# Performance work log

Measured on AMD Instinct MI355X. Metric: run time of the kernel, lower is better.

## Reference

```python
import jax, jax.numpy as jnp
import numpy as np

B, C, H, W = 16, 64, 64, 64
HD = 128


def skew(x):
    # x: [B,C,H,W] -> [B,C,H,H+W-1], row r shifted right by r
    b, c, h, w = x.shape
    sw = h + w - 1
    xp = jnp.pad(x, ((0, 0), (0, 0), (0, 0), (0, h - 1)))
    cols = (jnp.arange(sw)[None, :] - jnp.arange(h)[:, None]) % sw  # [H,SW]
    return xp[:, :, jnp.arange(h)[:, None], cols]


def unskew(x):
    # x: [B,C,H,SW] -> [B,C,H,W]
    b, c, h, sw = x.shape
    w = sw - h + 1
    cols = jnp.arange(w)[None, :] + jnp.arange(h)[:, None]  # [H,W]
    return x[:, :, jnp.arange(h)[:, None], cols]


def setup_inputs() -> dict:
    key = jax.random.key(0)
    k1, k2, k3, k4, k5 = jax.random.split(key, 5)
    s_is = 1.0 / np.sqrt(C)
    s_ss = 1.0 / np.sqrt(HD * 2)
    return {
        "x": jax.random.normal(k1, (B, C, H, W), jnp.float32),
        "w_is": jax.random.uniform(k2, (5 * HD, C), jnp.float32, -s_is, s_is),   # 1x1 conv (mask B, k=1 => plain)
        "b_is": jax.random.uniform(k3, (5 * HD,), jnp.float32, -s_is, s_is),
        "w_ss": jax.random.uniform(k4, (5 * HD, HD, 2), jnp.float32, -s_ss, s_ss),  # Conv1d k=2
        "b_ss": jax.random.uniform(k5, (5 * HD,), jnp.float32, -s_ss, s_ss),
    }


def reference(x, w_is, b_is, w_ss, b_ss):
    hd = w_ss.shape[1]
    sk = skew(x)  # [B,C,H,SW]
    # input-to-state: 1x1 conv over skewed map
    i_s = jnp.einsum("oc,bchw->bohw", w_is, sk) + b_is[None, :, None, None]
    is_cols = jnp.moveaxis(i_s, -1, 0)  # [SW,B,5hd,H]
    w0, w1 = w_ss[:, :, 0], w_ss[:, :, 1]  # taps for h[t-1], h[t]
    bsz, h_dim = x.shape[0], x.shape[2]

    def step(carry, ic):
        h_prev, c_prev = carry
        h_sh = jnp.pad(h_prev, ((0, 0), (0, 0), (1, 0)))[:, :, :-1]
        s_s = (jnp.einsum("oi,bih->boh", w1, h_prev)
               + jnp.einsum("oi,bih->boh", w0, h_sh)
               + b_ss[None, :, None])
        gates = ic + s_s
        o, fl, fu, i, g = jnp.split(gates, 5, axis=1)
        o, fl, fu, i = map(jax.nn.sigmoid, (o, fl, fu, i))
        g = jnp.tanh(g)
        c_sh = jnp.pad(c_prev, ((0, 0), (0, 0), (1, 0)))[:, :, :-1]
        c = fl * c_prev + fu * c_sh + i * g
        h = o * jnp.tanh(c)
        return (h, c), h

    z = jnp.zeros((bsz, hd, h_dim), x.dtype)
    _, hs = jax.lax.scan(step, (z, z), is_cols)
    hs = jnp.moveaxis(hs, 0, -1)  # [B,hd,H,SW]
    return unskew(hs)
```

## Files before the change

kernel.cpp:

```cpp
#include <hip/hip_runtime.h>

typedef __attribute__((ext_vector_type(8))) short bf16x8;
typedef __attribute__((ext_vector_type(4))) float f32x4;
typedef __attribute__((ext_vector_type(4))) uint  u32x4;

#define B_   16
#define C_   64
#define H_   64
#define W_   64
#define HD_  128
#define K_   320
#define SW_  127

#define NG    4
#define GH    32
#define NCG   64
#define TC    16
#define NT    640
#define ROWS  160
#define NKT   10
#define GPS   17

#define HSLOT  131072LL
#define CBX    524288LL
#define CNT    557056LL
#define GCNT   559104LL
#define AFB    561152LL
#define AF_N   204800LL
#define XT     765952LL
#define XT_N   4194304LL
#define WS_MIN (AFB + AF_N)
#define WS_XT  (XT + XT_N)

#define POLL_CAP (1 << 20)

__device__ __forceinline__ float sigm(float v) { return 1.f / (1.f + __expf(-v)); }
__device__ __forceinline__ float tanh_fast(float v) {
    float e = __expf(2.f * v);
    return 1.f - 2.f / (e + 1.f);
}

__device__ __forceinline__ int rload(int* p) {
    return __hip_atomic_load(p, __ATOMIC_RELAXED, __HIP_MEMORY_SCOPE_AGENT);
}
__device__ __forceinline__ void rbump(int* p) {
    __hip_atomic_fetch_add(p, 1, __ATOMIC_RELAXED, __HIP_MEMORY_SCOPE_AGENT);
}
__device__ __forceinline__ void wait_ge(int* p, int tgt) {
    int guard = 0;
    while (rload(p) < tgt) { if (++guard > POLL_CAP) break; }
    __atomic_signal_fence(__ATOMIC_ACQUIRE);
}

__device__ __forceinline__ void stu_nw(uint* p, uint v) {
    asm volatile("global_store_dword %0, %1, off sc0 sc1" :: "v"(p), "v"(v) : "memory");
}

__device__ __forceinline__ void poll2(const uint* p0, const uint* p1, uint want,
                                      u32x4& A, u32x4& B) {
    int guard = 0;
    while (true) {
        u32x4 a, b;
        asm volatile("global_load_dwordx4 %0, %2, off sc0 sc1\n\t"
                     "global_load_dwordx4 %1, %3, off sc0 sc1\n\t"
                     "s_waitcnt vmcnt(0)"
                     : "=&v"(a), "=&v"(b) : "v"(p0), "v"(p1) : "memory");
        uint m = a[0] & a[1] & a[2] & a[3] & b[0] & b[1] & b[2] & b[3];
        uint o = a[0] | a[1] | a[2] | a[3] | b[0] | b[1] | b[2] | b[3];
        bool ok = want ? ((m & 1u) != 0u) : ((o & 1u) == 0u);
        if (ok || ++guard > POLL_CAP) { A = a; B = b; return; }
    }
}
__device__ __forceinline__ void poll1(const uint* p, uint want, u32x4& A) {
    int guard = 0;
    while (true) {
        u32x4 a;
        asm volatile("global_load_dwordx4 %0, %1, off sc0 sc1\n\ts_waitcnt vmcnt(0)"
                     : "=&v"(a) : "v"(p) : "memory");
        uint m = a[0] & a[1] & a[2] & a[3];
        uint o = a[0] | a[1] | a[2] | a[3];
        bool ok = want ? ((m & 1u) != 0u) : ((o & 1u) == 0u);
        if (ok || ++guard > POLL_CAP) { A = a; return; }
    }
}

__device__ __forceinline__ uint bf16hi(uint u) { return (u + 0x7FFFu + ((u >> 16) & 1u)) >> 16; }
__device__ __forceinline__ uint2 splitbf(float v) {
    uint uh = bf16hi(__float_as_uint(v));
    float rl = v - __uint_as_float(uh << 16);
    uint ul = bf16hi(__float_as_uint(rl));
    return make_uint2(uh, ul);
}

__global__ void lstm_prep(const float* __restrict__ w_is,
                          const float* __restrict__ w_ss,
                          float* __restrict__ ws, long long n_ws)
{
    const long long stride = (long long)gridDim.x * blockDim.x;
    const long long t0 = (long long)blockIdx.x * blockDim.x + threadIdx.x;
    uint* wsu = (uint*)ws;

    for (long long i = t0; i < 524288LL + 32768LL; i += stride) {
        long long a = (i < 524288LL) ? i : (CBX + (i - 524288LL));
        stu_nw(wsu + a, 0x00000001u);
    }
    for (long long i = CNT + t0; i < CNT + 4096; i += stride)
        stu_nw(wsu + i, 0u);

    if (n_ws >= WS_MIN) {
        ushort* af = (ushort*)(ws + AFB);
        for (long long e = t0; e < AF_N; e += stride) {
            int idx   = (int)e;
            int chunk = idx >> 9;
            int lane  = (idx >> 3) & 63;
            int jj    = idx & 7;
            int g  = chunk / (10 * NKT);
            int rm = chunk % (10 * NKT);
            int rt = rm / NKT, kt = rm % NKT;
            int m = lane & 15, quad = lane >> 4;
            int r = rt * 16 + m;
            int q = r >> 5, hl = r & 31;
            int o = q * HD_ + g * GH + hl;
            int k = kt * 32 + quad * 8 + jj;
            float v;
            if (k < C_)            v = w_is[o * C_ + k];
            else if (k < C_ + HD_) v = w_ss[(o * HD_ + (k - C_)) * 2 + 1];
            else                   v = w_ss[(o * HD_ + (k - C_ - HD_)) * 2 + 0];
            uint uh = bf16hi(__float_as_uint(v));
            float rl = v - __uint_as_float(uh << 16);
            uint ul = bf16hi(__float_as_uint(rl));
            int base = chunk * 1024 + lane * 16 + jj;
            af[base]     = (ushort)uh;
            af[base + 8] = (ushort)ul;
        }
    }
}

__global__ void lstm_xpose(const float* __restrict__ x, float* __restrict__ ws)
{
    __shared__ float L[64 * 65];
    const int b = blockIdx.x >> 6, hr = blockIdx.x & 63;
    const int tid = threadIdx.x;
    #pragma unroll
    for (int it = 0; it < 16; ++it) {
        int c = it * 4 + (tid >> 6), w = tid & 63;
        L[c * 65 + w] = x[(((size_t)b * C_ + c) * H_ + hr) * W_ + w];
    }
    __syncthreads();
    float* xt = ws + XT;
    #pragma unroll
    for (int it = 0; it < 16; ++it) {
        int w = it * 4 + (tid >> 6), c = tid & 63;
        xt[(((size_t)b * H_ + hr) * W_ + w) * C_ + c] = L[c * 65 + w];
    }
}

__global__ void __launch_bounds__(NT, 3) lstm_persist(
    const float* __restrict__ x,
    const float* __restrict__ ws_c,
    const float* __restrict__ b_is,
    const float* __restrict__ b_ss,
    float* __restrict__ out,
    float* __restrict__ ws,
    int use_xt)
{
    __shared__ uint  Bf[NKT * 576];
    __shared__ float Gp[ROWS * GPS];
    __shared__ float Cs[2][17 * GH];
    __shared__ float bias_s[ROWS];

    const int tid = threadIdx.x;
    const int cgp = blockIdx.x >> 2;
    const int g   = blockIdx.x & 3;
    const int n0  = cgp * TC;
    const int inb  = (n0 & 63) != 0;
    const int hasr = ((n0 + TC) & 63) != 0;

    uint* hring = (uint*)ws;
    uint* cring = (uint*)(ws + CBX);
    int*  gcntp = (int*)(ws + GCNT);
    const float* xt = ws_c + XT;
    const uint4* afq = (const uint4*)(ws_c + AFB);

    if (tid < ROWS) {
        int q = tid >> 5, hl = tid & 31;
        int o = q * HD_ + g * GH + hl;
        bias_s[tid] = b_is[o] + b_ss[o];
    }
    if (tid < 17 * GH) Cs[0][tid] = 0.f;
    if (tid >= 544 && tid < 544 + GH) Cs[1][tid - 544] = 0.f;

    const int lane = tid & 63;
    const int wv   = tid >> 6;
    const int quad = lane >> 4;
    const int colc = lane & 15;
    uint* bfr = &Bf[lane * 8 + ((lane >> 2) << 2)];
    const uint4* ap0 = afq + (size_t)((g * 10 + wv) * NKT) * 128 + lane * 2;

    const int wkt = (wv < 8) ? (wv + 2) : (wv - 8);
    uint* wp = bfr + wkt * 576;
    int hn = 0, hd0 = 0, hskip = 0;
    if (wv < 8) {
        if (wv < 4) { hn = n0 + colc;     hd0 = wv * 32 + quad * 8; }
        else        { hn = n0 - 1 + colc; hd0 = (wv - 4) * 32 + quad * 8;
                      hskip = (colc == 0 && !inb); }
    }
    const int xc0 = (wv >= 8) ? ((wv - 8) * 32 + quad * 8) : 0;
    const int xn = n0 + colc, xb = xn >> 6, xhr = xn & 63;
    const int ii = tid - 512;

    bf16x8 Ahr[NKT], Alr[NKT];
    #pragma unroll
    for (int kt = 0; kt < NKT; ++kt) {
        uint4 ha = ap0[kt * 128];
        Ahr[kt] = *(bf16x8*)&ha;
        asm volatile("" : "+v"(Ahr[kt]));
        uint4 la = ap0[kt * 128 + 1];
        Alr[kt] = *(bf16x8*)&la;
        asm volatile("" : "+v"(Alr[kt]));
    }

    __syncthreads();

    for (int j = 0; j < SW_; ++j) {
        const uint want = ((j - 1) >> 2) & 1u;
        const uint wtag = (j >> 2) & 1u;

        if (wv < 8) {
            u32x4 a = {0, 0, 0, 0}, b = {0, 0, 0, 0};
            if (j > 0 && !hskip) {
                const uint* p = hring + (size_t)((j - 1) & 3) * HSLOT + hn * 128 + hd0;
                poll2(p, p + 4, want, a, b);
            }
            float hv8[8];
            #pragma unroll
            for (int r = 0; r < 4; ++r) {
                hv8[r]     = __uint_as_float(a[r]);
                hv8[4 + r] = __uint_as_float(b[r]);
            }
            uint hw[4], lw[4];
            #pragma unroll
            for (int p = 0; p < 4; ++p) {
                uint2 e0 = splitbf(hv8[2 * p]), e1 = splitbf(hv8[2 * p + 1]);
                hw[p] = e0.x | (e1.x << 16);
                lw[p] = e0.y | (e1.y << 16);
            }
            *(uint4*)wp       = make_uint4(hw[0], hw[1], hw[2], hw[3]);
            *(uint4*)(wp + 4) = make_uint4(lw[0], lw[1], lw[2], lw[3]);
        } else {
            float xv[8];
            int w = j - xhr;
            if ((unsigned)w < (unsigned)W_) {
                if (use_xt) {
                    const float* xp = xt + (((size_t)xb * H_ + xhr) * W_ + w) * C_ + xc0;
                    f32x4 va = *(const f32x4*)xp, vb = *(const f32x4*)(xp + 4);
                    #pragma unroll
                    for (int r = 0; r < 4; ++r) { xv[r] = va[r]; xv[4 + r] = vb[r]; }
                } else {
                    #pragma unroll
                    for (int r = 0; r < 8; ++r)
                        xv[r] = x[(((size_t)xb * C_ + xc0 + r) * H_ + xhr) * W_ + w];
                }
            } else {
                #pragma unroll
                for (int r = 0; r < 8; ++r) xv[r] = 0.f;
            }
            uint hw[4], lw[4];
            #pragma unroll
            for (int p = 0; p < 4; ++p) {
                uint2 e0 = splitbf(xv[2 * p]), e1 = splitbf(xv[2 * p + 1]);
                hw[p] = e0.x | (e1.x << 16);
                lw[p] = e0.y | (e1.y << 16);
            }
            *(uint4*)wp       = make_uint4(hw[0], hw[1], hw[2], hw[3]);
            *(uint4*)(wp + 4) = make_uint4(lw[0], lw[1], lw[2], lw[3]);

            if (ii >= 0 && ii < 8) {
                if (inb && j > 0) {
                    u32x4 cv;
                    const uint* cp = cring +
                        (((size_t)((j - 1) & 3) * NCG + (cgp - 1)) * NG + g) * GH + ii * 4;
                    poll1(cp, want, cv);
                    #pragma unroll
                    for (int r = 0; r < 4; ++r)
                        Cs[j & 1][ii * 4 + r] = __uint_as_float(cv[r]);
                }
            } else if (ii == 8) {
                if (j >= 4 && hasr) wait_ge(gcntp + (cgp + 1) * 32, 4 * (j - 2));
            }
        }
        __syncthreads();
        if (tid == 0) rbump(gcntp + cgp * 32);

        f32x4 acc = {0.f, 0.f, 0.f, 0.f};
        #pragma unroll
        for (int kt = 0; kt < NKT; ++kt) {
            const uint* bp = bfr + kt * 576;
            uint4 hb = *(const uint4*)bp;
            uint4 lb = *(const uint4*)(bp + 4);
            bf16x8 Bh = *(bf16x8*)&hb, Bl = *(bf16x8*)&lb;
            acc = __builtin_amdgcn_mfma_f32_16x16x32_bf16(Ahr[kt], Bh, acc, 0, 0, 0);
            acc = __builtin_amdgcn_mfma_f32_16x16x32_bf16(Ahr[kt], Bl, acc, 0, 0, 0);
            acc = __builtin_amdgcn_mfma_f32_16x16x32_bf16(Alr[kt], Bh, acc, 0, 0, 0);
            acc = __builtin_amdgcn_mfma_f32_16x16x32_bf16(Alr[kt], Bl, acc, 0, 0, 0);
        }
        #pragma unroll
        for (int r = 0; r < 4; ++r)
            Gp[(wv * 16 + quad * 4 + r) * GPS + colc] = acc[r];
        __syncthreads();

        if (tid < GH * TC) {
            const int hl = tid & 31, col = tid >> 5;
            int n = n0 + col, b = n >> 6, hr = n & 63;
            float go  = Gp[(0 * GH + hl) * GPS + col] + bias_s[0 * GH + hl];
            float gfl = Gp[(1 * GH + hl) * GPS + col] + bias_s[1 * GH + hl];
            float gfu = Gp[(2 * GH + hl) * GPS + col] + bias_s[2 * GH + hl];
            float gi  = Gp[(3 * GH + hl) * GPS + col] + bias_s[3 * GH + hl];
            float gg  = Gp[(4 * GH + hl) * GPS + col] + bias_s[4 * GH + hl];
            float so = sigm(go), sfl = sigm(gfl), sfu = sigm(gfu), si = sigm(gi);
            float tg = tanh_fast(gg);
            float cp = Cs[j & 1][(col + 1) * GH + hl];
            float cs = Cs[j & 1][col * GH + hl];
            float cv = sfl * cp + sfu * cs + si * tg;
            float hv = so * tanh_fast(cv);
            Cs[(j + 1) & 1][(col + 1) * GH + hl] = cv;

            uint pk = (__float_as_uint(hv) & ~1u) | wtag;
            stu_nw(hring + (size_t)(j & 3) * HSLOT + (size_t)n * 128 + g * GH + hl, pk);
            if (col == TC - 1) {
                uint cpk = (__float_as_uint(cv) & ~1u) | wtag;
                stu_nw(cring + (((size_t)(j & 3) * NCG + cgp) * NG + g) * GH + hl, cpk);
            }
            int w = j - hr;
            if ((unsigned)w < (unsigned)W_)
                out[(((size_t)b * HD_ + g * GH + hl) * H_ + hr) * W_ + w] = hv;
        }
    }
}

extern "C" void kernel_launch(void* const* d_in, const int* in_sizes, int n_in,
                              void* d_out, int out_size, void* d_ws, size_t ws_size,
                              hipStream_t stream)
{
    const float* x    = (const float*)d_in[0];
    const float* w_is = (const float*)d_in[1];
    const float* b_is = (const float*)d_in[2];
    const float* w_ss = (const float*)d_in[3];
    const float* b_ss = (const float*)d_in[4];
    float* out = (float*)d_out;
    float* ws  = (float*)d_ws;

    const long long n_ws = (long long)(ws_size / 4);
    const int use_xt = (n_ws >= WS_XT) ? 1 : 0;

    hipLaunchKernelGGL(lstm_prep, dim3(1024), dim3(256), 0, stream,
                       w_is, w_ss, ws, n_ws);
    if (use_xt)
        hipLaunchKernelGGL(lstm_xpose, dim3(B_ * H_), dim3(256), 0, stream, x, ws);

    hipLaunchKernelGGL(lstm_persist, dim3(NG * NCG), dim3(NT), 0, stream,
                       x, ws, b_is, b_ss, out, ws, use_xt);
}
```

Before: 579.6 us.

## Split h-ring polling across 17 column workers and dual-accumulate MFMA chain

Raises block size from 640 to 704 threads and reassigns roles. 544 threads each poll one 16-byte h chunk per column (17 columns including the left halo) and write it into two B-fragment slots, replacing the 8 waves that each polled two chunks. Separate thread ranges now handle x loading and the c-ring and neighbour-counter waits. The MFMA loop uses two interleaved accumulators under raised wave priority, and h stores are paired into dwordx2 writes via a lane shuffle. This aims to cut poll latency and the dependent MFMA chain per step, but launch_bounds drops from 3 to 2 blocks per SM, which changes occupancy and register limits.

```diff
diff --git a/kernel.cpp b/kernel.cpp
--- a/kernel.cpp
+++ b/kernel.cpp
@@ -3,6 +3,7 @@
 typedef __attribute__((ext_vector_type(8))) short bf16x8;
 typedef __attribute__((ext_vector_type(4))) float f32x4;
 typedef __attribute__((ext_vector_type(4))) uint  u32x4;
+typedef __attribute__((ext_vector_type(2))) uint  u32x2;
 
 #define B_   16
 #define C_   64
@@ -16,7 +17,7 @@
 #define GH    32
 #define NCG   64
 #define TC    16
-#define NT    640
+#define NT    704
 #define ROWS  160
 #define NKT   10
 #define GPS   17
@@ -55,22 +56,10 @@
 __device__ __forceinline__ void stu_nw(uint* p, uint v) {
     asm volatile("global_store_dword %0, %1, off sc0 sc1" :: "v"(p), "v"(v) : "memory");
 }
-
-__device__ __forceinline__ void poll2(const uint* p0, const uint* p1, uint want,
-                                      u32x4& A, u32x4& B) {
-    int guard = 0;
-    while (true) {
-        u32x4 a, b;
-        asm volatile("global_load_dwordx4 %0, %2, off sc0 sc1\n\t"
-                     "global_load_dwordx4 %1, %3, off sc0 sc1\n\t"
-                     "s_waitcnt vmcnt(0)"
-                     : "=&v"(a), "=&v"(b) : "v"(p0), "v"(p1) : "memory");
-        uint m = a[0] & a[1] & a[2] & a[3] & b[0] & b[1] & b[2] & b[3];
-        uint o = a[0] | a[1] | a[2] | a[3] | b[0] | b[1] | b[2] | b[3];
-        bool ok = want ? ((m & 1u) != 0u) : ((o & 1u) == 0u);
-        if (ok || ++guard > POLL_CAP) { A = a; B = b; return; }
-    }
-}
+__device__ __forceinline__ void st2_nw(uint* p, u32x2 v) {
+    asm volatile("global_store_dwordx2 %0, %1, off sc0 sc1" :: "v"(p), "v"(v) : "memory");
+}
+
 __device__ __forceinline__ void poll1(const uint* p, uint want, u32x4& A) {
     int guard = 0;
     while (true) {
@@ -155,7 +144,7 @@
     }
 }
 
-__global__ void __launch_bounds__(NT, 3) lstm_persist(
+__global__ void __launch_bounds__(NT, 2) lstm_persist(
     const float* __restrict__ x,
     const float* __restrict__ ws_c,
     const float* __restrict__ b_is,
@@ -195,29 +184,40 @@
     const int quad = lane >> 4;
     const int colc = lane & 15;
     uint* bfr = &Bf[lane * 8 + ((lane >> 2) << 2)];
-    const uint4* ap0 = afq + (size_t)((g * 10 + wv) * NKT) * 128 + lane * 2;
-
-    const int wkt = (wv < 8) ? (wv + 2) : (wv - 8);
-    uint* wp = bfr + wkt * 576;
-    int hn = 0, hd0 = 0, hskip = 0;
-    if (wv < 8) {
-        if (wv < 4) { hn = n0 + colc;     hd0 = wv * 32 + quad * 8; }
-        else        { hn = n0 - 1 + colc; hd0 = (wv - 4) * 32 + quad * 8;
-                      hskip = (colc == 0 && !inb); }
-    }
-    const int xc0 = (wv >= 8) ? ((wv - 8) * 32 + quad * 8) : 0;
-    const int xn = n0 + colc, xb = xn >> 6, xhr = xn & 63;
-    const int ii = tid - 512;
+
+    const int cp  = tid >> 5;
+    const int ch  = tid & 31;
+    const int pq  = (ch >> 1) & 3;
+    const int pj0 = (ch & 1) * 4;
+    const int kta = 2 + (ch >> 3);
+    const int laneA = pq * 16 + ((cp >= 1) ? (cp - 1) : 0);
+    const int laneB = pq * 16 + ((cp <= 15) ? cp : 0);
+    uint* bfA = &Bf[laneA * 8 + ((laneA >> 2) << 2) + kta * 576 + (pj0 >> 1)];
+    uint* bfB = &Bf[laneB * 8 + ((laneB >> 2) << 2) + (kta + 4) * 576 + (pj0 >> 1)];
+    const uint* hbase = hring + (size_t)(n0 - 1 + cp) * 128 + ch * 4;
+    const int pskip = (cp == 0 && !inb);
+
+    const int xi = tid - 544;
+    const int xkt = xi >> 6, xl = xi & 63;
+    const int xq = xl >> 4, xcolc = xl & 15;
+    const int xc0 = xkt * 32 + xq * 8;
+    const int xn = n0 + xcolc, xb = xn >> 6, xhr = xn & 63;
+    uint* bfX = &Bf[xl * 8 + ((xl >> 2) << 2) + xkt * 576];
+
+    const int ci = tid - 672;
 
     bf16x8 Ahr[NKT], Alr[NKT];
-    #pragma unroll
-    for (int kt = 0; kt < NKT; ++kt) {
-        uint4 ha = ap0[kt * 128];
-        Ahr[kt] = *(bf16x8*)&ha;
-        asm volatile("" : "+v"(Ahr[kt]));
-        uint4 la = ap0[kt * 128 + 1];
-        Alr[kt] = *(bf16x8*)&la;
-        asm volatile("" : "+v"(Alr[kt]));
+    if (wv < 10) {
+        const uint4* ap0 = afq + (size_t)((g * 10 + wv) * NKT) * 128 + lane * 2;
+        #pragma unroll
+        for (int kt = 0; kt < NKT; ++kt) {
+            uint4 ha = ap0[kt * 128];
+            Ahr[kt] = *(bf16x8*)&ha;
+            asm volatile("" : "+v"(Ahr[kt]));
+            uint4 la = ap0[kt * 128 + 1];
+            Alr[kt] = *(bf16x8*)&la;
+            asm volatile("" : "+v"(Alr[kt]));
+        }
     }
 
     __syncthreads();
@@ -226,28 +226,19 @@
         const uint want = ((j - 1) >> 2) & 1u;
         const uint wtag = (j >> 2) & 1u;
 
-        if (wv < 8) {
-            u32x4 a = {0, 0, 0, 0}, b = {0, 0, 0, 0};
-            if (j > 0 && !hskip) {
-                const uint* p = hring + (size_t)((j - 1) & 3) * HSLOT + hn * 128 + hd0;
-                poll2(p, p + 4, want, a, b);
-            }
-            float hv8[8];
-            #pragma unroll
-            for (int r = 0; r < 4; ++r) {
-                hv8[r]     = __uint_as_float(a[r]);
-                hv8[4 + r] = __uint_as_float(b[r]);
-            }
-            uint hw[4], lw[4];
-            #pragma unroll
-            for (int p = 0; p < 4; ++p) {
-                uint2 e0 = splitbf(hv8[2 * p]), e1 = splitbf(hv8[2 * p + 1]);
-                hw[p] = e0.x | (e1.x << 16);
-                lw[p] = e0.y | (e1.y << 16);
-            }
-            *(uint4*)wp       = make_uint4(hw[0], hw[1], hw[2], hw[3]);
-            *(uint4*)(wp + 4) = make_uint4(lw[0], lw[1], lw[2], lw[3]);
-        } else {
+        if (tid < 544) {
+            u32x4 a = {0, 0, 0, 0};
+            if (j > 0 && !pskip)
+                poll1(hbase + (size_t)((j - 1) & 3) * HSLOT, want, a);
+            uint2 e0 = splitbf(__uint_as_float(a[0]));
+            uint2 e1 = splitbf(__uint_as_float(a[1]));
+            uint2 e2 = splitbf(__uint_as_float(a[2]));
+            uint2 e3 = splitbf(__uint_as_float(a[3]));
+            u32x2 hp = {e0.x | (e1.x << 16), e2.x | (e3.x << 16)};
+            u32x2 lp = {e0.y | (e1.y << 16), e2.y | (e3.y << 16)};
+            if (cp >= 1)  { *(u32x2*)bfA = hp; *(u32x2*)(bfA + 4) = lp; }
+            if (cp <= 15) { *(u32x2*)bfB = hp; *(u32x2*)(bfB + 4) = lp; }
+        } else if (tid < 672) {
             float xv[8];
             int w = j - xhr;
             if ((unsigned)w < (unsigned)W_) {
@@ -272,41 +263,52 @@
                 hw[p] = e0.x | (e1.x << 16);
                 lw[p] = e0.y | (e1.y << 16);
             }
-            *(uint4*)wp       = make_uint4(hw[0], hw[1], hw[2], hw[3]);
-            *(uint4*)(wp + 4) = make_uint4(lw[0], lw[1], lw[2], lw[3]);
-
-            if (ii >= 0 && ii < 8) {
-                if (inb && j > 0) {
-                    u32x4 cv;
-                    const uint* cp = cring +
-                        (((size_t)((j - 1) & 3) * NCG + (cgp - 1)) * NG + g) * GH + ii * 4;
-                    poll1(cp, want, cv);
-                    #pragma unroll
-                    for (int r = 0; r < 4; ++r)
-                        Cs[j & 1][ii * 4 + r] = __uint_as_float(cv[r]);
-                }
-            } else if (ii == 8) {
-                if (j >= 4 && hasr) wait_ge(gcntp + (cgp + 1) * 32, 4 * (j - 2));
-            }
+            *(uint4*)bfX       = make_uint4(hw[0], hw[1], hw[2], hw[3]);
+            *(uint4*)(bfX + 4) = make_uint4(lw[0], lw[1], lw[2], lw[3]);
+        } else if (ci >= 0 && ci < 8) {
+            if (inb && j > 0) {
+                u32x4 cv;
+                const uint* cpx = cring +
+                    (((size_t)((j - 1) & 3) * NCG + (cgp - 1)) * NG + g) * GH + ci * 4;
+                poll1(cpx, want, cv);
+                #pragma unroll
+                for (int r = 0; r < 4; ++r)
+                    Cs[j & 1][ci * 4 + r] = __uint_as_float(cv[r]);
+            }
+        } else if (ci == 8) {
+            if (j >= 4 && hasr) wait_ge(gcntp + (cgp + 1) * 32, 4 * (j - 2));
         }
         __syncthreads();
         if (tid == 0) rbump(gcntp + cgp * 32);
 
-        f32x4 acc = {0.f, 0.f, 0.f, 0.f};
-        #pragma unroll
-        for (int kt = 0; kt < NKT; ++kt) {
-            const uint* bp = bfr + kt * 576;
-            uint4 hb = *(const uint4*)bp;
-            uint4 lb = *(const uint4*)(bp + 4);
-            bf16x8 Bh = *(bf16x8*)&hb, Bl = *(bf16x8*)&lb;
-            acc = __builtin_amdgcn_mfma_f32_16x16x32_bf16(Ahr[kt], Bh, acc, 0, 0, 0);
-            acc = __builtin_amdgcn_mfma_f32_16x16x32_bf16(Ahr[kt], Bl, acc, 0, 0, 0);
-            acc = __builtin_amdgcn_mfma_f32_16x16x32_bf16(Alr[kt], Bh, acc, 0, 0, 0);
-            acc = __builtin_amdgcn_mfma_f32_16x16x32_bf16(Alr[kt], Bl, acc, 0, 0, 0);
-        }
-        #pragma unroll
-        for (int r = 0; r < 4; ++r)
-            Gp[(wv * 16 + quad * 4 + r) * GPS + colc] = acc[r];
+        if (wv < 10) {
+            f32x4 acc0 = {0.f, 0.f, 0.f, 0.f};
+            f32x4 acc1 = {0.f, 0.f, 0.f, 0.f};
+            __builtin_amdgcn_s_setprio(1);
+            #pragma unroll
+            for (int kt = 0; kt < NKT; kt += 2) {
+                const uint* bp0 = bfr + kt * 576;
+                uint4 hb0 = *(const uint4*)bp0;
+                uint4 lb0 = *(const uint4*)(bp0 + 4);
+                const uint* bp1 = bfr + (kt + 1) * 576;
+                uint4 hb1 = *(const uint4*)bp1;
+                uint4 lb1 = *(const uint4*)(bp1 + 4);
+                bf16x8 Bh0 = *(bf16x8*)&hb0, Bl0 = *(bf16x8*)&lb0;
+                bf16x8 Bh1 = *(bf16x8*)&hb1, Bl1 = *(bf16x8*)&lb1;
+                acc0 = __builtin_amdgcn_mfma_f32_16x16x32_bf16(Ahr[kt],     Bh0, acc0, 0, 0, 0);
+                acc1 = __builtin_amdgcn_mfma_f32_16x16x32_bf16(Ahr[kt + 1], Bh1, acc1, 0, 0, 0);
+                acc0 = __builtin_amdgcn_mfma_f32_16x16x32_bf16(Ahr[kt],     Bl0, acc0, 0, 0, 0);
+                acc1 = __builtin_amdgcn_mfma_f32_16x16x32_bf16(Ahr[kt + 1], Bl1, acc1, 0, 0, 0);
+                acc0 = __builtin_amdgcn_mfma_f32_16x16x32_bf16(Alr[kt],     Bh0, acc0, 0, 0, 0);
+                acc1 = __builtin_amdgcn_mfma_f32_16x16x32_bf16(Alr[kt + 1], Bh1, acc1, 0, 0, 0);
+                acc0 = __builtin_amdgcn_mfma_f32_16x16x32_bf16(Alr[kt],     Bl0, acc0, 0, 0, 0);
+                acc1 = __builtin_amdgcn_mfma_f32_16x16x32_bf16(Alr[kt + 1], Bl1, acc1, 0, 0, 0);
+            }
+            __builtin_amdgcn_s_setprio(0);
+            #pragma unroll
+            for (int r = 0; r < 4; ++r)
+                Gp[(wv * 16 + quad * 4 + r) * GPS + colc] = acc0[r] + acc1[r];
+        }
         __syncthreads();
 
         if (tid < GH * TC) {
@@ -319,14 +321,18 @@
             float gg  = Gp[(4 * GH + hl) * GPS + col] + bias_s[4 * GH + hl];
             float so = sigm(go), sfl = sigm(gfl), sfu = sigm(gfu), si = sigm(gi);
             float tg = tanh_fast(gg);
-            float cp = Cs[j & 1][(col + 1) * GH + hl];
+            float cp_ = Cs[j & 1][(col + 1) * GH + hl];
             float cs = Cs[j & 1][col * GH + hl];
-            float cv = sfl * cp + sfu * cs + si * tg;
+            float cv = sfl * cp_ + sfu * cs + si * tg;
             float hv = so * tanh_fast(cv);
             Cs[(j + 1) & 1][(col + 1) * GH + hl] = cv;
 
             uint pk = (__float_as_uint(hv) & ~1u) | wtag;
-            stu_nw(hring + (size_t)(j & 3) * HSLOT + (size_t)n * 128 + g * GH + hl, pk);
+            uint other = (uint)__shfl_xor((int)pk, 1);
+            if (!(hl & 1)) {
+                u32x2 pv = {pk, other};
+                st2_nw(hring + (size_t)(j & 3) * HSLOT + (size_t)n * 128 + g * GH + (hl & ~1), pv);
+            }
             if (col == TC - 1) {
                 uint cpk = (__float_as_uint(cv) & ~1u) | wtag;
                 stu_nw(cring + (((size_t)(j & 3) * NCG + cgp) * NG + g) * GH + hl, cpk);
```

Result: faster. 496.1 us (-14.4%).
